# Kernel optimization log

Hardware: AMD Instinct MI355X
Metric: run time of the kernel (lower is better)

The kernel has to match this reference:

```python
import jax, jax.numpy as jnp
import numpy as np

DIM = 20
N = 200000
E = 6400000
ITERATIONS = 3


def setup_inputs() -> dict:
    key = jax.random.key(0)
    ks = jax.random.split(key, 20)
    inp = {
        "h": jax.random.normal(ks[0], (N, DIM), dtype=jnp.float32),
        "node2depth": jax.random.randint(ks[1], (N,), 0, 5, dtype=jnp.int32),
        "edge_src": jax.random.randint(ks[2], (E,), 0, N, dtype=jnp.int32),
        "edge_dst": jax.random.randint(ks[3], (E,), 0, N, dtype=jnp.int32),
    }
    # Six DIM x DIM Linear layers (weight stored [out,in] like torch, plus bias)
    scale = 1.0 / np.sqrt(DIM)
    names = ["Wz", "Uz", "Wr", "Ur", "Wh", "Uh"]
    for j, nm in enumerate(names):
        inp[nm + "_w"] = jax.random.uniform(ks[4 + 2 * j], (DIM, DIM), jnp.float32, -scale, scale)
        inp[nm + "_b"] = jax.random.uniform(ks[5 + 2 * j], (DIM,), jnp.float32, -scale, scale)
    return inp


def _linear(x, w, b):
    return x @ w.T + b


def reference(h, Wz_w, Wz_b, Uz_w, Uz_b, Wr_w, Wr_b, Ur_w, Ur_b,
              Wh_w, Wh_b, Uh_w, Uh_b, node2depth, edge_src, edge_dst):
    active = None
    for i in range(ITERATIONS):
        # active set shrinks as i grows (depth + i <= ITERATIONS)
        active = (node2depth + i) <= ITERATIONS  # [N] bool
        af = active.astype(h.dtype)
        # x[u] = sum over neighbors v of h[v], counting only active src AND active dst
        msg = h[edge_src] * af[edge_src][:, None]          # [E, DIM]
        x = jax.ops.segment_sum(msg, edge_dst, num_segments=N)  # [N, DIM]
        x = x * af[:, None]
        z = jax.nn.sigmoid(_linear(x, Wz_w, Wz_b) + _linear(h, Uz_w, Uz_b))
        r = jax.nn.sigmoid(_linear(x, Wr_w, Wr_b) + _linear(h, Ur_w, Ur_b))
        h_cand = jnp.tanh(_linear(x, Wh_w, Wh_b) + _linear(r * h, Uh_w, Uh_b))
        h_new = z * h + (1.0 - z) * h_cand
        # inactive nodes are dropped from the dict in the original; since the
        # active set only shrinks, keeping their old h is equivalent
        h = jnp.where(active[:, None], h_new, h)
    # original returns only nodes active at the last iteration; zero out the rest
    return jnp.where(active[:, None], h, jnp.zeros_like(h))
```

## Files before the change

### kernel.cpp

```cpp
#include <hip/hip_runtime.h>

#define DIM    20
#define NN     200000
#define EE     6400000
#define ITERS  3
#define BLOCK  256

#define NODES_PER_FINE   64
#define NFINE            3125
#define NCOARSE          98
#define FINE_PER_COARSE  32
#define TILE             4096
#define IPT              16

typedef unsigned int u32;

__global__ __launch_bounds__(BLOCK) void k1_count(const int* __restrict__ edst,
                                                  const int* __restrict__ depth,
                                                  int* __restrict__ fine_cnt,
                                                  int* __restrict__ dcnt) {
    __shared__ u32 lhist[NFINE];
    __shared__ u32 dh[5];
    int tid = threadIdx.x;
    for (int i = tid; i < NFINE; i += BLOCK) lhist[i] = 0;
    if (tid < 5) dh[tid] = 0;
    __syncthreads();
    for (int e = blockIdx.x * BLOCK + tid; e < EE; e += gridDim.x * BLOCK) {
        int d = edst[e];
        atomicAdd(&lhist[d >> 6], 1u);
    }
    for (int n = blockIdx.x * BLOCK + tid; n < NN; n += gridDim.x * BLOCK) {
        atomicAdd(&dh[depth[n]], 1u);
    }
    __syncthreads();
    for (int i = tid; i < NFINE; i += BLOCK) {
        u32 v = lhist[i];
        if (v) atomicAdd((u32*)&fine_cnt[i], v);
    }
    if (tid < 5) dcnt[tid * 256 + blockIdx.x] = (int)dh[tid];
}

__global__ __launch_bounds__(BLOCK) void k2_scan(const int* __restrict__ fine_cnt,
                                                 int* __restrict__ fine_base,
                                                 int* __restrict__ fine_cursor,
                                                 int* __restrict__ coarse_base,
                                                 int* __restrict__ coarse_cursor,
                                                 const int* __restrict__ dcnt,
                                                 int* __restrict__ dbase,
                                                 int* __restrict__ cum) {
    __shared__ int wsum[4];
    __shared__ int sdb[1281];
    int tid = threadIdx.x;
    int lane = tid & 63, wid = tid >> 6;

    {
        const int CH = 13;
        int loc[CH];
        int base = tid * CH;
        int s = 0;
        #pragma unroll
        for (int j = 0; j < CH; ++j) {
            int idx = base + j;
            int v = (idx < NFINE) ? fine_cnt[idx] : 0;
            loc[j] = v; s += v;
        }
        int incl = s;
        #pragma unroll
        for (int off = 1; off < 64; off <<= 1) {
            int t = __shfl_up(incl, off, 64);
            if (lane >= off) incl += t;
        }
        if (lane == 63) wsum[wid] = incl;
        __syncthreads();
        int woff = 0;
        for (int w = 0; w < wid; ++w) woff += wsum[w];
        int run = woff + incl - s;
        #pragma unroll
        for (int j = 0; j < CH; ++j) {
            int idx = base + j;
            if (idx < NFINE) {
                fine_base[idx]   = run;
                fine_cursor[idx] = run;
                run += loc[j];
            }
        }
        if (tid == 0) fine_base[NFINE] = EE;
        __syncthreads();
        if (tid < NCOARSE + 1) {
            int f = tid * FINE_PER_COARSE; if (f > NFINE) f = NFINE;
            int v = fine_base[f];
            coarse_base[tid] = v;
            if (tid < NCOARSE) coarse_cursor[tid] = v;
        }
    }
    __syncthreads();

    {
        const int CH2 = 5;
        int loc[CH2];
        int base = tid * CH2;
        int s = 0;
        #pragma unroll
        for (int j = 0; j < CH2; ++j) { int v = dcnt[base + j]; loc[j] = v; s += v; }
        int incl = s;
        #pragma unroll
        for (int off = 1; off < 64; off <<= 1) {
            int t = __shfl_up(incl, off, 64);
            if (lane >= off) incl += t;
        }
        if (lane == 63) wsum[wid] = incl;
        __syncthreads();
        int woff = 0;
        for (int w = 0; w < wid; ++w) woff += wsum[w];
        int run = woff + incl - s;
        #pragma unroll
        for (int j = 0; j < CH2; ++j) {
            sdb[base + j]   = run;
            dbase[base + j] = run;
            run += loc[j];
        }
        if (tid == 255) sdb[1280] = run;
        __syncthreads();
        if (tid < 5) cum[tid] = sdb[(tid + 1) * 256];
    }
}

__global__ __launch_bounds__(BLOCK) void kd_scatter(const int* __restrict__ depth,
                                                    const int* __restrict__ dbase,
                                                    int* __restrict__ perm) {
    __shared__ u32 dh[5];
    int tid = threadIdx.x;
    if (tid < 5) dh[tid] = 0;
    __syncthreads();
    for (int n = blockIdx.x * BLOCK + tid; n < NN; n += gridDim.x * BLOCK) {
        int d = depth[n];
        u32 r = atomicAdd(&dh[d], 1u);
        perm[n] = dbase[d * 256 + blockIdx.x] + (int)r;
    }
}

__global__ __launch_bounds__(BLOCK) void p1_split(const int* __restrict__ esrc,
                                                  const int* __restrict__ edst,
                                                  const int* __restrict__ perm,
                                                  int* __restrict__ coarse_cursor,
                                                  u32* __restrict__ buf1) {
    __shared__ u32 lhist[NCOARSE];
    __shared__ u32 gbase[NCOARSE];
    int tid = threadIdx.x;
    int start = blockIdx.x * TILE;
    if (tid < NCOARSE) lhist[tid] = 0;
    __syncthreads();

    u32 item[IPT]; u32 key[IPT]; u32 rank[IPT];
    #pragma unroll
    for (int k = 0; k < IPT; ++k) {
        int e = start + k * BLOCK + tid;
        if (e < EE) {
            int d = edst[e];
            int s = esrc[e];
            u32 pid = (u32)perm[s];
            u32 c = (u32)d >> 11;
            key[k]  = c;
            item[k] = ((u32)d & 2047u) | (pid << 11);
            rank[k] = atomicAdd(&lhist[c], 1u);
        }
    }
    __syncthreads();
    if (tid < NCOARSE) {
        u32 cnt = lhist[tid];
        gbase[tid] = cnt ? (u32)atomicAdd((u32*)&coarse_cursor[tid], cnt) : 0u;
    }
    __syncthreads();
    #pragma unroll
    for (int k = 0; k < IPT; ++k) {
        int e = start + k * BLOCK + tid;
        if (e < EE) buf1[gbase[key[k]] + rank[k]] = item[k];
    }
}

__global__ __launch_bounds__(BLOCK) void p2_split(const u32* __restrict__ buf1,
                                                  const int* __restrict__ coarse_base,
                                                  int* __restrict__ fine_cursor,
                                                  u32* __restrict__ buf2) {
    __shared__ u32 lhist[2 * FINE_PER_COARSE];
    __shared__ u32 gbase[2 * FINE_PER_COARSE];
    __shared__ int cb[NCOARSE + 1];
    __shared__ int sc0;
    int tid = threadIdx.x;
    int start = blockIdx.x * TILE;
    if (tid < NCOARSE + 1) cb[tid] = coarse_base[tid];
    if (tid < 2 * FINE_PER_COARSE) { lhist[tid] = 0; gbase[tid] = 0; }
    __syncthreads();
    if (tid == 0) {
        int c = 0;
        while (c + 1 < NCOARSE && cb[c + 1] <= start) ++c;
        sc0 = c;
    }
    __syncthreads();
    int c0 = sc0;
    int b1 = cb[c0 + 1];

    u32 item[IPT]; u32 key[IPT]; u32 rank[IPT];
    #pragma unroll
    for (int k = 0; k < IPT; ++k) {
        int i = start + k * BLOCK + tid;
        if (i < EE) {
            u32 w = buf1[i];
            u32 dlow = w & 2047u;
            u32 pid  = w >> 11;
            u32 kk = ((i < b1) ? 0u : (u32)FINE_PER_COARSE) + (dlow >> 6);
            key[k]  = kk;
            item[k] = (dlow & 63u) | (pid << 6);
            rank[k] = atomicAdd(&lhist[kk], 1u);
        }
    }
    __syncthreads();
    if (tid < 2 * FINE_PER_COARSE) {
        u32 cnt = lhist[tid];
        int idx = c0 * FINE_PER_COARSE + tid;
        if (cnt && idx < NFINE)
            gbase[tid] = (u32)atomicAdd((u32*)&fine_cursor[idx], cnt);
    }
    __syncthreads();
    #pragma unroll
    for (int k = 0; k < IPT; ++k) {
        int i = start + k * BLOCK + tid;
        if (i < EE) buf2[gbase[key[k]] + rank[k]] = item[k];
    }
}

__global__ __launch_bounds__(BLOCK) void pb_sort(const u32* __restrict__ buf2,
                                                 const int* __restrict__ fine_base,
                                                 const int* __restrict__ cum,
                                                 int* __restrict__ ptr,
                                                 u32* __restrict__ cnt3,
                                                 u32* __restrict__ ssrc) {
    __shared__ u32 hist[512];
    __shared__ u32 ebase[512];
    __shared__ u32 lout[TILE];
    __shared__ u32 wsum[4];
    int tid = threadIdx.x;
    int b = blockIdx.x;
    int lo = fine_base[b];
    int hi = fine_base[b + 1];
    int cnt = hi - lo;
    u32 c0 = (u32)cum[0], c1 = (u32)cum[1], c2 = (u32)cum[2], c3 = (u32)cum[3];
    hist[tid] = 0; hist[tid + 256] = 0;
    __syncthreads();

    u32 item[IPT]; u32 key[IPT]; u32 rank[IPT];
    #pragma unroll
    for (int k = 0; k < IPT; ++k) {
        int i = lo + k * BLOCK + tid;
        if (i < hi) {
            u32 w = buf2[i];
            u32 pid = w >> 6;
            u32 dep = (u32)(pid >= c0) + (u32)(pid >= c1)
                    + (u32)(pid >= c2) + (u32)(pid >= c3);
            u32 kk = (w & 63u) * 8u + dep;
            key[k]  = kk;
            item[k] = pid;
            rank[k] = atomicAdd(&hist[kk], 1u);
        }
    }
    __syncthreads();
    {
        u32 s0 = hist[2 * tid], s1 = hist[2 * tid + 1];
        u32 s = s0 + s1;
        int lane = tid & 63, wid = tid >> 6;
        u32 incl = s;
        #pragma unroll
        for (int off = 1; off < 64; off <<= 1) {
            u32 t = __shfl_up((int)incl, off, 64);
            if (lane >= off) incl += t;
        }
        if (lane == 63) wsum[wid] = incl;
        __syncthreads();
        u32 woff = 0;
        for (int w = 0; w < wid; ++w) woff += wsum[w];
        u32 excl = woff + incl - s;
        ebase[2 * tid]     = excl;
        ebase[2 * tid + 1] = excl + s0;
    }
    __syncthreads();
    if (tid < NODES_PER_FINE) {
        u32 base0 = ebase[tid * 8];
        u32 cc1 = ebase[tid * 8 + 2] - base0;
        u32 cc2 = ebase[tid * 8 + 3] - base0;
        u32 cc3 = ebase[tid * 8 + 4] - base0;
        int u = b * NODES_PER_FINE + tid;
        ptr[u]  = lo + (int)base0;
        cnt3[u] = cc1 | (cc2 << 10) | (cc3 << 20);
    }
    #pragma unroll
    for (int k = 0; k < IPT; ++k) {
        int i = lo + k * BLOCK + tid;
        if (i < hi) lout[ebase[key[k]] + rank[k]] = item[k];
    }
    __syncthreads();
    for (int j = tid; j < cnt; j += BLOCK) ssrc[lo + j] = lout[j];
}

__device__ __forceinline__ u32 pack_bf16x2(float a, float b) {
    u32 ua = __float_as_uint(a);
    u32 ub = __float_as_uint(b);
    ua = (ua + 0x7FFFu + ((ua >> 16) & 1u)) >> 16;
    ub = (ub + 0x7FFFu + ((ub >> 16) & 1u)) & 0xFFFF0000u;
    return ua | ub;
}

__global__ __launch_bounds__(BLOCK) void hconv(const float* __restrict__ h,
                                               u32* __restrict__ hb,
                                               const int* __restrict__ perm,
                                               const int* __restrict__ depth) {
    int g = blockIdx.x * BLOCK + threadIdx.x;
    if (g >= NN * 16) return;
    int node = g >> 4, slot = g & 15;
    if (slot >= 10) return;
    if (depth[node] > ITERS) return;
    float2 f = *(const float2*)(h + (size_t)node * DIM + slot * 2);
    hb[(size_t)perm[node] * 16 + slot] = pack_bf16x2(f.x, f.y);
}


__device__ __forceinline__ float bl(u32 w) { return __uint_as_float(w << 16); }
__device__ __forceinline__ float bh(u32 w) { return __uint_as_float(w & 0xFFFF0000u); }

__device__ __forceinline__ void acc_bf16row(float* x, uint4 A, uint4 B, uint2 C) {
    x[0]+=bl(A.x);  x[1]+=bh(A.x);  x[2]+=bl(A.y);  x[3]+=bh(A.y);
    x[4]+=bl(A.z);  x[5]+=bh(A.z);  x[6]+=bl(A.w);  x[7]+=bh(A.w);
    x[8]+=bl(B.x);  x[9]+=bh(B.x);  x[10]+=bl(B.y); x[11]+=bh(B.y);
    x[12]+=bl(B.z); x[13]+=bh(B.z); x[14]+=bl(B.w); x[15]+=bh(B.w);
    x[16]+=bl(C.x); x[17]+=bh(C.x); x[18]+=bl(C.y); x[19]+=bh(C.y);
}

__global__ __launch_bounds__(BLOCK) void gather_x(
    const u32* __restrict__ hb,
    const int* __restrict__ depth, const int* __restrict__ ptr,
    const u32* __restrict__ cnt3, const u32* __restrict__ ssrc,
    float* __restrict__ xg, int lim, int shift)
{
    int tid = threadIdx.x;
    int u = blockIdx.x * 32 + (tid >> 3);
    int t = tid & 7;
    if (depth[u] > lim) return;
    int p = ptr[u];
    int d = (int)((cnt3[u] >> shift) & 1023u);
    float x[DIM];
    #pragma unroll
    for (int k = 0; k < DIM; ++k) x[k] = 0.0f;

    int e = t;
    for (; e + 8 < d; e += 16) {
        u32 v0 = ssrc[p + e];
        u32 v1 = ssrc[p + e + 8];
        const u32* r0 = hb + (size_t)v0 * 16;
        const u32* r1 = hb + (size_t)v1 * 16;
        uint4 A0 = *(const uint4*)r0; uint4 B0 = *(const uint4*)(r0 + 4);
        uint2 C0 = *(const uint2*)(r0 + 8);
        uint4 A1 = *(const uint4*)r1; uint4 B1 = *(const uint4*)(r1 + 4);
        uint2 C1 = *(const uint2*)(r1 + 8);
        acc_bf16row(x, A0, B0, C0);
        acc_bf16row(x, A1, B1, C1);
    }
    if (e < d) {
        u32 v0 = ssrc[p + e];
        const u32* r0 = hb + (size_t)v0 * 16;
        uint4 A0 = *(const uint4*)r0; uint4 B0 = *(const uint4*)(r0 + 4);
        uint2 C0 = *(const uint2*)(r0 + 8);
        acc_bf16row(x, A0, B0, C0);
    }
    #pragma unroll
    for (int k = 0; k < DIM; ++k) {
        x[k] += __shfl_xor(x[k], 1, 64);
        x[k] += __shfl_xor(x[k], 2, 64);
        x[k] += __shfl_xor(x[k], 4, 64);
    }
    float* xr = xg + (size_t)u * DIM;
    xr[t]     = x[t];
    xr[t + 8] = x[t + 8];
    if (t < 4) xr[t + 16] = x[t + 16];
}


__device__ __forceinline__ float fast_sigmoid(float t) {
    return 1.0f / (1.0f + __expf(-t));
}
__device__ __forceinline__ float fast_tanh(float t) {
    t = fminf(fmaxf(t, -15.0f), 15.0f);
    float e2 = __expf(2.0f * t);
    return (e2 - 1.0f) / (e2 + 1.0f);
}

__global__ __launch_bounds__(BLOCK) void gru_update(
    const float* __restrict__ xg,
    const float* __restrict__ h_in, float* __restrict__ h_out,
    u32* __restrict__ hb_out,
    const int* __restrict__ depth, const int* __restrict__ perm,
    const int* __restrict__ cum,
    const float* __restrict__ Wz, const float* __restrict__ bWz,
    const float* __restrict__ Uz, const float* __restrict__ bUz,
    const float* __restrict__ Wr, const float* __restrict__ bWr,
    const float* __restrict__ Ur, const float* __restrict__ bUr,
    const float* __restrict__ Wh, const float* __restrict__ bWh,
    const float* __restrict__ Uh, const float* __restrict__ bUh,
    int lim, int cumIdx, int isFinal)
{
    int u = blockIdx.x * BLOCK + threadIdx.x;
    if (u >= NN) return;
    bool act = depth[u] <= lim;
    if (!act) {
        if (isFinal) {
            float4 z4 = make_float4(0.f, 0.f, 0.f, 0.f);
            float4* o4 = (float4*)(h_out + (size_t)u * DIM);
            #pragma unroll
            for (int q = 0; q < 5; ++q) o4[q] = z4;
        }
        return;
    }

    float x[DIM], h[DIM];
    {
        const float4* xv = (const float4*)(xg + (size_t)u * DIM);
        float4 a0 = xv[0], a1 = xv[1], a2 = xv[2], a3 = xv[3], a4 = xv[4];
        x[0]=a0.x; x[1]=a0.y; x[2]=a0.z; x[3]=a0.w;
        x[4]=a1.x; x[5]=a1.y; x[6]=a1.z; x[7]=a1.w;
        x[8]=a2.x; x[9]=a2.y; x[10]=a2.z; x[11]=a2.w;
        x[12]=a3.x; x[13]=a3.y; x[14]=a3.z; x[15]=a3.w;
        x[16]=a4.x; x[17]=a4.y; x[18]=a4.z; x[19]=a4.w;
    }
    {
        const float4* hv = (const float4*)(h_in + (size_t)u * DIM);
        float4 a0 = hv[0], a1 = hv[1], a2 = hv[2], a3 = hv[3], a4 = hv[4];
        h[0]=a0.x; h[1]=a0.y; h[2]=a0.z; h[3]=a0.w;
        h[4]=a1.x; h[5]=a1.y; h[6]=a1.z; h[7]=a1.w;
        h[8]=a2.x; h[9]=a2.y; h[10]=a2.z; h[11]=a2.w;
        h[12]=a3.x; h[13]=a3.y; h[14]=a3.z; h[15]=a3.w;
        h[16]=a4.x; h[17]=a4.y; h[18]=a4.z; h[19]=a4.w;
    }

    float z[DIM], rh[DIM];
    #pragma unroll
    for (int j = 0; j < DIM; ++j) {
        float sz = bWz[j] + bUz[j];
        float sr = bWr[j] + bUr[j];
        #pragma unroll
        for (int k = 0; k < DIM; ++k) {
            sz += x[k] * Wz[j * DIM + k];
            sz += h[k] * Uz[j * DIM + k];
            sr += x[k] * Wr[j * DIM + k];
            sr += h[k] * Ur[j * DIM + k];
        }
        z[j]  = fast_sigmoid(sz);
        rh[j] = fast_sigmoid(sr) * h[j];
    }

    float o[DIM];
    #pragma unroll
    for (int j = 0; j < DIM; ++j) {
        float sh = bWh[j] + bUh[j];
        #pragma unroll
        for (int k = 0; k < DIM; ++k) {
            sh += x[k]  * Wh[j * DIM + k];
            sh += rh[k] * Uh[j * DIM + k];
        }
        float hc = fast_tanh(sh);
        o[j] = z[j] * h[j] + (1.0f - z[j]) * hc;
    }

    {
        float4* o4 = (float4*)(h_out + (size_t)u * DIM);
        o4[0] = make_float4(o[0],  o[1],  o[2],  o[3]);
        o4[1] = make_float4(o[4],  o[5],  o[6],  o[7]);
        o4[2] = make_float4(o[8],  o[9],  o[10], o[11]);
        o4[3] = make_float4(o[12], o[13], o[14], o[15]);
        o4[4] = make_float4(o[16], o[17], o[18], o[19]);
    }
    if (!isFinal) {
        int pid = perm[u];
        if (pid < cum[cumIdx]) {
            u32* row = hb_out + (size_t)pid * 16;
            uint4 wA = make_uint4(pack_bf16x2(o[0], o[1]),  pack_bf16x2(o[2], o[3]),
                                  pack_bf16x2(o[4], o[5]),  pack_bf16x2(o[6], o[7]));
            uint4 wB = make_uint4(pack_bf16x2(o[8], o[9]),  pack_bf16x2(o[10], o[11]),
                                  pack_bf16x2(o[12], o[13]), pack_bf16x2(o[14], o[15]));
            uint2 wC = make_uint2(pack_bf16x2(o[16], o[17]), pack_bf16x2(o[18], o[19]));
            *(uint4*)row       = wA;
            *(uint4*)(row + 4) = wB;
            *(uint2*)(row + 8) = wC;
        }
    }
}


extern "C" void kernel_launch(void* const* d_in, const int* in_sizes, int n_in,
                              void* d_out, int out_size, void* d_ws, size_t ws_size,
                              hipStream_t stream) {
    const float* h0    = (const float*)d_in[0];
    const int*   depth = (const int*)d_in[1];
    const int*   esrc  = (const int*)d_in[2];
    const int*   edst  = (const int*)d_in[3];
    const float* Wz  = (const float*)d_in[4];  const float* bWz = (const float*)d_in[5];
    const float* Uz  = (const float*)d_in[6];  const float* bUz = (const float*)d_in[7];
    const float* Wr  = (const float*)d_in[8];  const float* bWr = (const float*)d_in[9];
    const float* Ur  = (const float*)d_in[10]; const float* bUr = (const float*)d_in[11];
    const float* Wh  = (const float*)d_in[12]; const float* bWh = (const float*)d_in[13];
    const float* Uh  = (const float*)d_in[14]; const float* bUh = (const float*)d_in[15];
    float* out = (float*)d_out;

    int* W = (int*)d_ws;
    int*  fine_cnt      = W + 0;
    int*  fine_base     = W + 3200;
    int*  fine_cursor   = W + 6400;
    int*  coarse_base   = W + 9600;
    int*  coarse_cursor = W + 9728;
    int*  dcnt          = W + 9856;
    int*  dbase         = W + 11200;
    int*  cum           = W + 12544;
    int*  ptr           = W + 12800;
    u32*  cnt3          = (u32*)(W + 212864);
    int*  perm          = W + 412864;
    u32*  buf1          = (u32*)(W + 612864);
    u32*  buf2          = buf1 + EE;
    float* h1           = (float*)(buf2 + EE);
    u32*  hb            = (u32*)(h1 + (size_t)NN * DIM);
    u32*  ssrc          = buf1;
    float* xg           = (float*)buf2;

    hipMemsetAsync(fine_cnt, 0, NFINE * sizeof(int), stream);

    int ntile = (EE + TILE - 1) / TILE;

    k1_count  <<<256, BLOCK, 0, stream>>>(edst, depth, fine_cnt, dcnt);
    k2_scan   <<<1,   BLOCK, 0, stream>>>(fine_cnt, fine_base, fine_cursor,
                                          coarse_base, coarse_cursor, dcnt, dbase, cum);
    kd_scatter<<<256, BLOCK, 0, stream>>>(depth, dbase, perm);
    p1_split  <<<ntile, BLOCK, 0, stream>>>(esrc, edst, perm, coarse_cursor, buf1);
    p2_split  <<<ntile, BLOCK, 0, stream>>>(buf1, coarse_base, fine_cursor, buf2);
    pb_sort   <<<NFINE, BLOCK, 0, stream>>>(buf2, fine_base, cum, ptr, cnt3, ssrc);
    hconv     <<<(NN * 16) / BLOCK, BLOCK, 0, stream>>>(h0, hb, perm, depth);

    gather_x  <<<NN / 32, BLOCK, 0, stream>>>(hb, depth, ptr, cnt3, ssrc, xg, 3, 20);
    gru_update<<<(NN + BLOCK - 1) / BLOCK, BLOCK, 0, stream>>>(xg, h0, h1, hb, depth, perm, cum,
        Wz, bWz, Uz, bUz, Wr, bWr, Ur, bUr, Wh, bWh, Uh, bUh, 3, 2, 0);
    gather_x  <<<NN / 32, BLOCK, 0, stream>>>(hb, depth, ptr, cnt3, ssrc, xg, 2, 10);
    gru_update<<<(NN + BLOCK - 1) / BLOCK, BLOCK, 0, stream>>>(xg, h1, h1, hb, depth, perm, cum,
        Wz, bWz, Uz, bUz, Wr, bWr, Ur, bUr, Wh, bWh, Uh, bUh, 2, 1, 0);
    gather_x  <<<NN / 32, BLOCK, 0, stream>>>(hb, depth, ptr, cnt3, ssrc, xg, 1, 0);
    gru_update<<<(NN + BLOCK - 1) / BLOCK, BLOCK, 0, stream>>>(xg, h1, out, hb, depth, perm, cum,
        Wz, bWz, Uz, bUz, Wr, bWr, Ur, bUr, Wh, bWh, Uh, bUh, 1, 0, 1);
}
```

Baseline: 541.1 us.

## Single-pass fine binning and split bf16 hidden-state layout for gather

Replaces the two-pass coarse/fine radix split of edges with one pass that bins directly into 3125 fine buckets using a 512-thread block and a large shared histogram, removing one full read/write of the edge buffer. The bf16 hidden-state copy is also split into a 32-byte main array and an 8-byte tail array, so it no longer uses a padded 64-byte row. In the gather, each neighbor row is now loaded by two lanes instead of one, which changes the reduction pattern. The single-pass binning adds heavy shared-memory atomics and much more global scatter fragmentation across many buckets.

Measured after the change: 549.1 us. Within noise of the previous version (+1.5%).

```diff
diff --git a/kernel.cpp b/kernel.cpp
--- a/kernel.cpp
+++ b/kernel.cpp
@@ -8,10 +8,12 @@
 
 #define NODES_PER_FINE   64
 #define NFINE            3125
-#define NCOARSE          98
-#define FINE_PER_COARSE  32
 #define TILE             4096
 #define IPT              16
+
+#define BLOCK2 512
+#define IPT2   16
+#define TILE2  (BLOCK2 * IPT2)
 
 typedef unsigned int u32;
 
@@ -43,8 +45,6 @@
 __global__ __launch_bounds__(BLOCK) void k2_scan(const int* __restrict__ fine_cnt,
                                                  int* __restrict__ fine_base,
                                                  int* __restrict__ fine_cursor,
-                                                 int* __restrict__ coarse_base,
-                                                 int* __restrict__ coarse_cursor,
                                                  const int* __restrict__ dcnt,
                                                  int* __restrict__ dbase,
                                                  int* __restrict__ cum) {
@@ -85,13 +85,6 @@
             }
         }
         if (tid == 0) fine_base[NFINE] = EE;
-        __syncthreads();
-        if (tid < NCOARSE + 1) {
-            int f = tid * FINE_PER_COARSE; if (f > NFINE) f = NFINE;
-            int v = fine_base[f];
-            coarse_base[tid] = v;
-            if (tid < NCOARSE) coarse_cursor[tid] = v;
-        }
     }
     __syncthreads();
 
@@ -139,93 +132,42 @@
     }
 }
 
-__global__ __launch_bounds__(BLOCK) void p1_split(const int* __restrict__ esrc,
-                                                  const int* __restrict__ edst,
-                                                  const int* __restrict__ perm,
-                                                  int* __restrict__ coarse_cursor,
-                                                  u32* __restrict__ buf1) {
-    __shared__ u32 lhist[NCOARSE];
-    __shared__ u32 gbase[NCOARSE];
+__global__ __launch_bounds__(BLOCK2) void p1_bin(const int* __restrict__ esrc,
+                                                 const int* __restrict__ edst,
+                                                 const int* __restrict__ perm,
+                                                 int* __restrict__ fine_cursor,
+                                                 u32* __restrict__ buf2) {
+    __shared__ u32 lhist[NFINE];
+    __shared__ u32 gbase[NFINE];
     int tid = threadIdx.x;
-    int start = blockIdx.x * TILE;
-    if (tid < NCOARSE) lhist[tid] = 0;
-    __syncthreads();
-
-    u32 item[IPT]; u32 key[IPT]; u32 rank[IPT];
-    #pragma unroll
-    for (int k = 0; k < IPT; ++k) {
-        int e = start + k * BLOCK + tid;
+    int start = blockIdx.x * TILE2;
+    for (int i = tid; i < NFINE; i += BLOCK2) lhist[i] = 0;
+    __syncthreads();
+
+    u32 item[IPT2]; u32 key[IPT2]; u32 rank[IPT2];
+    #pragma unroll
+    for (int k = 0; k < IPT2; ++k) {
+        int e = start + k * BLOCK2 + tid;
         if (e < EE) {
             int d = edst[e];
             int s = esrc[e];
             u32 pid = (u32)perm[s];
-            u32 c = (u32)d >> 11;
-            key[k]  = c;
-            item[k] = ((u32)d & 2047u) | (pid << 11);
-            rank[k] = atomicAdd(&lhist[c], 1u);
-        }
-    }
-    __syncthreads();
-    if (tid < NCOARSE) {
-        u32 cnt = lhist[tid];
-        gbase[tid] = cnt ? (u32)atomicAdd((u32*)&coarse_cursor[tid], cnt) : 0u;
-    }
-    __syncthreads();
-    #pragma unroll
-    for (int k = 0; k < IPT; ++k) {
-        int e = start + k * BLOCK + tid;
-        if (e < EE) buf1[gbase[key[k]] + rank[k]] = item[k];
-    }
-}
-
-__global__ __launch_bounds__(BLOCK) void p2_split(const u32* __restrict__ buf1,
-                                                  const int* __restrict__ coarse_base,
-                                                  int* __restrict__ fine_cursor,
-                                                  u32* __restrict__ buf2) {
-    __shared__ u32 lhist[2 * FINE_PER_COARSE];
-    __shared__ u32 gbase[2 * FINE_PER_COARSE];
-    __shared__ int cb[NCOARSE + 1];
-    __shared__ int sc0;
-    int tid = threadIdx.x;
-    int start = blockIdx.x * TILE;
-    if (tid < NCOARSE + 1) cb[tid] = coarse_base[tid];
-    if (tid < 2 * FINE_PER_COARSE) { lhist[tid] = 0; gbase[tid] = 0; }
-    __syncthreads();
-    if (tid == 0) {
-        int c = 0;
-        while (c + 1 < NCOARSE && cb[c + 1] <= start) ++c;
-        sc0 = c;
-    }
-    __syncthreads();
-    int c0 = sc0;
-    int b1 = cb[c0 + 1];
-
-    u32 item[IPT]; u32 key[IPT]; u32 rank[IPT];
-    #pragma unroll
-    for (int k = 0; k < IPT; ++k) {
-        int i = start + k * BLOCK + tid;
-        if (i < EE) {
-            u32 w = buf1[i];
-            u32 dlow = w & 2047u;
-            u32 pid  = w >> 11;
-            u32 kk = ((i < b1) ? 0u : (u32)FINE_PER_COARSE) + (dlow >> 6);
+            u32 kk = (u32)d >> 6;
             key[k]  = kk;
-            item[k] = (dlow & 63u) | (pid << 6);
+            item[k] = ((u32)d & 63u) | (pid << 6);
             rank[k] = atomicAdd(&lhist[kk], 1u);
         }
     }
     __syncthreads();
-    if (tid < 2 * FINE_PER_COARSE) {
-        u32 cnt = lhist[tid];
-        int idx = c0 * FINE_PER_COARSE + tid;
-        if (cnt && idx < NFINE)
-            gbase[tid] = (u32)atomicAdd((u32*)&fine_cursor[idx], cnt);
-    }
-    __syncthreads();
-    #pragma unroll
-    for (int k = 0; k < IPT; ++k) {
-        int i = start + k * BLOCK + tid;
-        if (i < EE) buf2[gbase[key[k]] + rank[k]] = item[k];
+    for (int i = tid; i < NFINE; i += BLOCK2) {
+        u32 c = lhist[i];
+        gbase[i] = c ? (u32)atomicAdd((u32*)&fine_cursor[i], c) : 0u;
+    }
+    __syncthreads();
+    #pragma unroll
+    for (int k = 0; k < IPT2; ++k) {
+        int e = start + k * BLOCK2 + tid;
+        if (e < EE) buf2[gbase[key[k]] + rank[k]] = item[k];
     }
 }
 
@@ -310,76 +252,90 @@
 }
 
 __global__ __launch_bounds__(BLOCK) void hconv(const float* __restrict__ h,
-                                               u32* __restrict__ hb,
+                                               u32* __restrict__ hbA,
+                                               u32* __restrict__ hbC,
                                                const int* __restrict__ perm,
                                                const int* __restrict__ depth) {
     int g = blockIdx.x * BLOCK + threadIdx.x;
-    if (g >= NN * 16) return;
-    int node = g >> 4, slot = g & 15;
-    if (slot >= 10) return;
+    if (g >= NN * 8) return;
+    int node = g >> 3, s = g & 7;
     if (depth[node] > ITERS) return;
-    float2 f = *(const float2*)(h + (size_t)node * DIM + slot * 2);
-    hb[(size_t)perm[node] * 16 + slot] = pack_bf16x2(f.x, f.y);
+    int pid = perm[node];
+    float2 f = *(const float2*)(h + (size_t)node * DIM + s * 2);
+    hbA[(size_t)pid * 8 + s] = pack_bf16x2(f.x, f.y);
+    if (s < 2) {
+        float2 fc = *(const float2*)(h + (size_t)node * DIM + 16 + s * 2);
+        hbC[(size_t)pid * 2 + s] = pack_bf16x2(fc.x, fc.y);
+    }
 }
 
 
 __device__ __forceinline__ float bl(u32 w) { return __uint_as_float(w << 16); }
 __device__ __forceinline__ float bh(u32 w) { return __uint_as_float(w & 0xFFFF0000u); }
 
-__device__ __forceinline__ void acc_bf16row(float* x, uint4 A, uint4 B, uint2 C) {
-    x[0]+=bl(A.x);  x[1]+=bh(A.x);  x[2]+=bl(A.y);  x[3]+=bh(A.y);
-    x[4]+=bl(A.z);  x[5]+=bh(A.z);  x[6]+=bl(A.w);  x[7]+=bh(A.w);
-    x[8]+=bl(B.x);  x[9]+=bh(B.x);  x[10]+=bl(B.y); x[11]+=bh(B.y);
-    x[12]+=bl(B.z); x[13]+=bh(B.z); x[14]+=bl(B.w); x[15]+=bh(B.w);
-    x[16]+=bl(C.x); x[17]+=bh(C.x); x[18]+=bl(C.y); x[19]+=bh(C.y);
+__device__ __forceinline__ void acc_half(float* xa, float* xc, uint4 a, u32 c) {
+    xa[0]+=bl(a.x); xa[1]+=bh(a.x);
+    xa[2]+=bl(a.y); xa[3]+=bh(a.y);
+    xa[4]+=bl(a.z); xa[5]+=bh(a.z);
+    xa[6]+=bl(a.w); xa[7]+=bh(a.w);
+    xc[0]+=bl(c);   xc[1]+=bh(c);
 }
 
 __global__ __launch_bounds__(BLOCK) void gather_x(
-    const u32* __restrict__ hb,
+    const u32* __restrict__ hbA, const u32* __restrict__ hbC,
     const int* __restrict__ depth, const int* __restrict__ ptr,
     const u32* __restrict__ cnt3, const u32* __restrict__ ssrc,
     float* __restrict__ xg, int lim, int shift)
 {
     int tid = threadIdx.x;
     int u = blockIdx.x * 32 + (tid >> 3);
-    int t = tid & 7;
+    int j = tid & 7;
+    int r = j >> 1;
+    int q = j & 1;
     if (depth[u] > lim) return;
     int p = ptr[u];
     int d = (int)((cnt3[u] >> shift) & 1023u);
-    float x[DIM];
-    #pragma unroll
-    for (int k = 0; k < DIM; ++k) x[k] = 0.0f;
-
-    int e = t;
-    for (; e + 8 < d; e += 16) {
-        u32 v0 = ssrc[p + e];
-        u32 v1 = ssrc[p + e + 8];
-        const u32* r0 = hb + (size_t)v0 * 16;
-        const u32* r1 = hb + (size_t)v1 * 16;
-        uint4 A0 = *(const uint4*)r0; uint4 B0 = *(const uint4*)(r0 + 4);
-        uint2 C0 = *(const uint2*)(r0 + 8);
-        uint4 A1 = *(const uint4*)r1; uint4 B1 = *(const uint4*)(r1 + 4);
-        uint2 C1 = *(const uint2*)(r1 + 8);
-        acc_bf16row(x, A0, B0, C0);
-        acc_bf16row(x, A1, B1, C1);
+
+    float xa[8], xc[2];
+    #pragma unroll
+    for (int k = 0; k < 8; ++k) xa[k] = 0.0f;
+    xc[0] = 0.0f; xc[1] = 0.0f;
+
+    int e = r;
+    for (; e + 4 < d; e += 8) {
+        u32 pid0 = ssrc[p + e];
+        u32 pid1 = ssrc[p + e + 4];
+        uint4 a0 = *(const uint4*)(hbA + (size_t)pid0 * 8 + q * 4);
+        u32   c0 = hbC[(size_t)pid0 * 2 + q];
+        uint4 a1 = *(const uint4*)(hbA + (size_t)pid1 * 8 + q * 4);
+        u32   c1 = hbC[(size_t)pid1 * 2 + q];
+        acc_half(xa, xc, a0, c0);
+        acc_half(xa, xc, a1, c1);
     }
     if (e < d) {
-        u32 v0 = ssrc[p + e];
-        const u32* r0 = hb + (size_t)v0 * 16;
-        uint4 A0 = *(const uint4*)r0; uint4 B0 = *(const uint4*)(r0 + 4);
-        uint2 C0 = *(const uint2*)(r0 + 8);
-        acc_bf16row(x, A0, B0, C0);
-    }
-    #pragma unroll
-    for (int k = 0; k < DIM; ++k) {
-        x[k] += __shfl_xor(x[k], 1, 64);
-        x[k] += __shfl_xor(x[k], 2, 64);
-        x[k] += __shfl_xor(x[k], 4, 64);
-    }
+        u32 pid0 = ssrc[p + e];
+        uint4 a0 = *(const uint4*)(hbA + (size_t)pid0 * 8 + q * 4);
+        u32   c0 = hbC[(size_t)pid0 * 2 + q];
+        acc_half(xa, xc, a0, c0);
+    }
+    #pragma unroll
+    for (int k = 0; k < 8; ++k) {
+        xa[k] += __shfl_xor(xa[k], 2, 64);
+        xa[k] += __shfl_xor(xa[k], 4, 64);
+    }
+    xc[0] += __shfl_xor(xc[0], 2, 64); xc[0] += __shfl_xor(xc[0], 4, 64);
+    xc[1] += __shfl_xor(xc[1], 2, 64); xc[1] += __shfl_xor(xc[1], 4, 64);
+
     float* xr = xg + (size_t)u * DIM;
-    xr[t]     = x[t];
-    xr[t + 8] = x[t + 8];
-    if (t < 4) xr[t + 16] = x[t + 16];
+    if (j == 0) {
+        *(float4*)(xr)      = make_float4(xa[0], xa[1], xa[2], xa[3]);
+        *(float4*)(xr + 4)  = make_float4(xa[4], xa[5], xa[6], xa[7]);
+        *(float2*)(xr + 16) = make_float2(xc[0], xc[1]);
+    } else if (j == 1) {
+        *(float4*)(xr + 8)  = make_float4(xa[0], xa[1], xa[2], xa[3]);
+        *(float4*)(xr + 12) = make_float4(xa[4], xa[5], xa[6], xa[7]);
+        *(float2*)(xr + 18) = make_float2(xc[0], xc[1]);
+    }
 }
 
 
@@ -395,7 +351,7 @@
 __global__ __launch_bounds__(BLOCK) void gru_update(
     const float* __restrict__ xg,
     const float* __restrict__ h_in, float* __restrict__ h_out,
-    u32* __restrict__ hb_out,
+    u32* __restrict__ hbA, u32* __restrict__ hbC,
     const int* __restrict__ depth, const int* __restrict__ perm,
     const int* __restrict__ cum,
     const float* __restrict__ Wz, const float* __restrict__ bWz,
@@ -479,15 +435,15 @@
     if (!isFinal) {
         int pid = perm[u];
         if (pid < cum[cumIdx]) {
-            u32* row = hb_out + (size_t)pid * 16;
-            uint4 wA = make_uint4(pack_bf16x2(o[0], o[1]),  pack_bf16x2(o[2], o[3]),
-                                  pack_bf16x2(o[4], o[5]),  pack_bf16x2(o[6], o[7]));
-            uint4 wB = make_uint4(pack_bf16x2(o[8], o[9]),  pack_bf16x2(o[10], o[11]),
-                                  pack_bf16x2(o[12], o[13]), pack_bf16x2(o[14], o[15]));
-            uint2 wC = make_uint2(pack_bf16x2(o[16], o[17]), pack_bf16x2(o[18], o[19]));
-            *(uint4*)row       = wA;
-            *(uint4*)(row + 4) = wB;
-            *(uint2*)(row + 8) = wC;
+            u32* rowA = hbA + (size_t)pid * 8;
+            uint4 wA0 = make_uint4(pack_bf16x2(o[0], o[1]),   pack_bf16x2(o[2], o[3]),
+                                   pack_bf16x2(o[4], o[5]),   pack_bf16x2(o[6], o[7]));
+            uint4 wA1 = make_uint4(pack_bf16x2(o[8], o[9]),   pack_bf16x2(o[10], o[11]),
+                                   pack_bf16x2(o[12], o[13]), pack_bf16x2(o[14], o[15]));
+            *(uint4*)rowA       = wA0;
+            *(uint4*)(rowA + 4) = wA1;
+            *(uint2*)(hbC + (size_t)pid * 2) =
+                make_uint2(pack_bf16x2(o[16], o[17]), pack_bf16x2(o[18], o[19]));
         }
     }
 }
@@ -512,41 +468,39 @@
     int*  fine_cnt      = W + 0;
     int*  fine_base     = W + 3200;
     int*  fine_cursor   = W + 6400;
-    int*  coarse_base   = W + 9600;
-    int*  coarse_cursor = W + 9728;
-    int*  dcnt          = W + 9856;
-    int*  dbase         = W + 11200;
-    int*  cum           = W + 12544;
+    int*  dcnt          = W + 9600;
+    int*  dbase         = W + 10880;
+    int*  cum           = W + 12160;
     int*  ptr           = W + 12800;
     u32*  cnt3          = (u32*)(W + 212864);
     int*  perm          = W + 412864;
     u32*  buf1          = (u32*)(W + 612864);
     u32*  buf2          = buf1 + EE;
     float* h1           = (float*)(buf2 + EE);
-    u32*  hb            = (u32*)(h1 + (size_t)NN * DIM);
+    u32*  hbA           = (u32*)(h1 + (size_t)NN * DIM);
+    u32*  hbC           = hbA + (size_t)NN * 8;
     u32*  ssrc          = buf1;
     float* xg           = (float*)buf2;
 
     hipMemsetAsync(fine_cnt, 0, NFINE * sizeof(int), stream);
 
-    int ntile = (EE + TILE - 1) / TILE;
+    int nt2 = (EE + TILE2 - 1) / TILE2;
 
     k1_count  <<<256, BLOCK, 0, stream>>>(edst, depth, fine_cnt, dcnt);
     k2_scan   <<<1,   BLOCK, 0, stream>>>(fine_cnt, fine_base, fine_cursor,
-                                          coarse_base, coarse_cursor, dcnt, dbase, cum);
+                                          dcnt, dbase, cum);
     kd_scatter<<<256, BLOCK, 0, stream>>>(depth, dbase, perm);
-    p1_split  <<<ntile, BLOCK, 0, stream>>>(esrc, edst, perm, coarse_cursor, buf1);
-    p2_split  <<<ntile, BLOCK, 0, stream>>>(buf1, coarse_base, fine_cursor, buf2);
+    p1_bin    <<<nt2, BLOCK2, 0, stream>>>(esrc, edst, perm, fine_cursor, buf2);
     pb_sort   <<<NFINE, BLOCK, 0, stream>>>(buf2, fine_base, cum, ptr, cnt3, ssrc);
-    hconv     <<<(NN * 16) / BLOCK, BLOCK, 0, stream>>>(h0, hb, perm, depth);
-
-    gather_x  <<<NN / 32, BLOCK, 0, stream>>>(hb, depth, ptr, cnt3, ssrc, xg, 3, 20);
-    gru_update<<<(NN + BLOCK - 1) / BLOCK, BLOCK, 0, stream>>>(xg, h0, h1, hb, depth, perm, cum,
+    hconv     <<<(NN * 8) / BLOCK, BLOCK, 0, stream>>>(h0, hbA, hbC, perm, depth);
+
+    gather_x  <<<NN / 32, BLOCK, 0, stream>>>(hbA, hbC, depth, ptr, cnt3, ssrc, xg, 3, 20);
+    gru_update<<<(NN + BLOCK - 1) / BLOCK, BLOCK, 0, stream>>>(xg, h0, h1, hbA, hbC, depth, perm, cum,
         Wz, bWz, Uz, bUz, Wr, bWr, Ur, bUr, Wh, bWh, Uh, bUh, 3, 2, 0);
-    gather_x  <<<NN / 32, BLOCK, 0, stream>>>(hb, depth, ptr, cnt3, ssrc, xg, 2, 10);
-    gru_update<<<(NN + BLOCK - 1) / BLOCK, BLOCK, 0, stream>>>(xg, h1, h1, hb, depth, perm, cum,
+    gather_x  <<<NN / 32, BLOCK, 0, stream>>>(hbA, hbC, depth, ptr, cnt3, ssrc, xg, 2, 10);
+    gru_update<<<(NN + BLOCK - 1) / BLOCK, BLOCK, 0, stream>>>(xg, h1, h1, hbA, hbC, depth, perm, cum,
         Wz, bWz, Uz, bUz, Wr, bWr, Ur, bUr, Wh, bWh, Uh, bUh, 2, 1, 0);
-    gather_x  <<<NN / 32, BLOCK, 0, stream>>>(hb, depth, ptr, cnt3, ssrc, xg, 1, 0);
-    gru_update<<<(NN + BLOCK - 1) / BLOCK, BLOCK, 0, stream>>>(xg, h1, out, hb, depth, perm, cum,
+    gather_x  <<<NN / 32, BLOCK, 0, stream>>>(hbA, hbC, depth, ptr, cnt3, ssrc, xg, 1, 0);
+    gru_update<<<(NN + BLOCK - 1) / BLOCK, BLOCK, 0, stream>>>(xg, h1, out, hbA, hbC, depth, perm, cum,
         Wz, bWz, Uz, bUz, Wr, bWr, Ur, bUr, Wh, bWh, Uh, bUh, 1, 0, 1);
 }
```
